# Optimization experiments

Hardware: AMD Instinct MI355X
Metric: run time of the kernel (lower is better)

Reference implementation:

```python
import jax, jax.numpy as jnp
import numpy as np

MARGIN = 0.3
EPS = 1e-8  # torch CosineSimilarity eps


def setup_inputs() -> dict:
    key = jax.random.key(0)
    k1, k2 = jax.random.split(key)
    x = jax.random.normal(k1, (8192, 1024), dtype=jnp.float32)
    y = jax.random.normal(k2, (8192, 1024), dtype=jnp.float32)
    return {"x": x, "y": y}


def _rank(S):
    # S[i, j] = cos(a_i, b_j); positives on the diagonal.
    d = jnp.diagonal(S)                      # [N] positive similarities
    E = jnp.exp(S)                           # [N, N]
    neg = jnp.sum(E, axis=1) - jnp.exp(d)    # sum over j != i of exp(S[i, j])
    m1 = jnp.exp(d - MARGIN)
    ret = -jnp.log(m1 / (m1 + neg))          # per-anchor AMS loss
    return jnp.mean(ret)


def reference(x, y):
    xn = x / jnp.maximum(jnp.linalg.norm(x, axis=-1, keepdims=True), EPS)
    yn = y / jnp.maximum(jnp.linalg.norm(y, axis=-1, keepdims=True), EPS)
    S = xn @ yn.T                            # [N, N] full cosine-similarity matrix
    # calculate_loss = rank(x, y) + rank(y, x); rank(y, x) uses S.T
    return _rank(S) + _rank(S.T)
```

## Files before the change

### kernel.cpp

```cpp
#include <hip/hip_runtime.h>
#include <hip/hip_bf16.h>
#include <math.h>

#define NROWS 8192
#define DDIM  1024
#define BT    128
#define BKB   128
#define MARGIN 0.3f
#define INV256 0.00390625f

typedef __attribute__((ext_vector_type(4))) float  f32x4;
typedef __attribute__((ext_vector_type(8))) __bf16 bf16x8;
typedef __attribute__((ext_vector_type(4))) int    i32x4;
typedef __attribute__((ext_vector_type(8))) int    i32x8;

__device__ __forceinline__ unsigned f2bf_bits(float f) {
  unsigned u = __float_as_uint(f);
  u += 0x7fffu + ((u >> 16) & 1u);
  return u >> 16;
}

__global__ __launch_bounds__(256) void normconv8_kernel(const float* __restrict__ x,
                                                        const float* __restrict__ y,
                                                        unsigned int* __restrict__ xq,
                                                        unsigned int* __restrict__ yq,
                                                        float* __restrict__ zero_base) {
  if (blockIdx.x < 16) {
    ((float4*)zero_base)[blockIdx.x * 256 + threadIdx.x] = (float4){0.f, 0.f, 0.f, 0.f};
  }
  int wid  = blockIdx.x * 4 + (threadIdx.x >> 6);
  int lane = threadIdx.x & 63;
  const float* src;
  unsigned int* dst;
  int row;
  if (wid < NROWS) { src = x; dst = xq; row = wid; }
  else             { src = y; dst = yq; row = wid - NROWS; }
  const float4* p = (const float4*)(src + (size_t)row * DDIM);
  float4 v[4];
  float s = 0.f;
#pragma unroll
  for (int a = 0; a < 4; ++a) {
    v[a] = p[a * 64 + lane];
    s = fmaf(v[a].x, v[a].x, s); s = fmaf(v[a].y, v[a].y, s);
    s = fmaf(v[a].z, v[a].z, s); s = fmaf(v[a].w, v[a].w, s);
  }
#pragma unroll
  for (int m = 1; m < 64; m <<= 1) s += __shfl_xor(s, m, 64);
  float inv = 16.0f / fmaxf(sqrtf(s), 1e-8f);
  unsigned int* d4 = dst + (size_t)row * (DDIM / 4);
#pragma unroll
  for (int a = 0; a < 4; ++a) {
    int w = __builtin_amdgcn_cvt_pk_fp8_f32(v[a].x * inv, v[a].y * inv, 0, false);
    w     = __builtin_amdgcn_cvt_pk_fp8_f32(v[a].z * inv, v[a].w * inv, w, true);
    d4[a * 64 + lane] = (unsigned int)w;
  }
}

__global__ __launch_bounds__(256) void gemm_mx_kernel(const unsigned char* __restrict__ xq,
                                                      const unsigned char* __restrict__ yq,
                                                      float* __restrict__ rowsum,
                                                      float* __restrict__ colsum,
                                                      float* __restrict__ diagv) {
  __shared__ alignas(16) unsigned char As[BT * BKB];
  __shared__ alignas(16) unsigned char Bs[BT * BKB];
  __shared__ float red_row[BT];
  __shared__ float red_col[BT];

  const int tid  = threadIdx.x;
  const int bi   = blockIdx.y;
  const int bj   = blockIdx.x;
  const int lane = tid & 63;
  const int wave = tid >> 6;
  const int wr   = wave >> 1, wc = wave & 1;
  const int quad = lane >> 4, l15 = lane & 15;

  if (tid < BT) red_row[tid] = 0.f; else red_col[tid - BT] = 0.f;

  const int r_l = lane >> 3;
  const int cg  = (lane & 7) ^ r_l;
  const unsigned char* ga = xq + (size_t)(bi * BT + wave * 32 + r_l) * DDIM + cg * 16;
  const unsigned char* gb = yq + (size_t)(bj * BT + wave * 32 + r_l) * DDIM + cg * 16;

  f32x4 acc[4][4];
#pragma unroll
  for (int i = 0; i < 4; ++i)
#pragma unroll
    for (int j = 0; j < 4; ++j) acc[i][j] = (f32x4){0.f, 0.f, 0.f, 0.f};

  const int r7 = l15 & 7;
  for (int k0 = 0; k0 < DDIM; k0 += BKB) {
#pragma unroll
    for (int a = 0; a < 4; ++a) {
      __builtin_amdgcn_global_load_lds(
          (const __attribute__((address_space(1))) unsigned int*)(ga + (size_t)a * 8 * DDIM + k0),
          (__attribute__((address_space(3))) unsigned int*)&As[(wave * 32 + a * 8) * BKB],
          16, 0, 0);
      __builtin_amdgcn_global_load_lds(
          (const __attribute__((address_space(1))) unsigned int*)(gb + (size_t)a * 8 * DDIM + k0),
          (__attribute__((address_space(3))) unsigned int*)&Bs[(wave * 32 + a * 8) * BKB],
          16, 0, 0);
    }
    __syncthreads();
    i32x8 af[4], bf[4];
#pragma unroll
    for (int f = 0; f < 4; ++f) {
      const unsigned char* ra = &As[(wr * 64 + f * 16 + l15) * BKB];
      const unsigned char* rb = &Bs[(wc * 64 + f * 16 + l15) * BKB];
      i32x4 alo = *(const i32x4*)(ra + (((quad * 2 + 0) ^ r7) * 16));
      i32x4 ahi = *(const i32x4*)(ra + (((quad * 2 + 1) ^ r7) * 16));
      i32x4 blo = *(const i32x4*)(rb + (((quad * 2 + 0) ^ r7) * 16));
      i32x4 bhi = *(const i32x4*)(rb + (((quad * 2 + 1) ^ r7) * 16));
      af[f] = (i32x8){alo.x, alo.y, alo.z, alo.w, ahi.x, ahi.y, ahi.z, ahi.w};
      bf[f] = (i32x8){blo.x, blo.y, blo.z, blo.w, bhi.x, bhi.y, bhi.z, bhi.w};
    }
#pragma unroll
    for (int fr = 0; fr < 4; ++fr)
#pragma unroll
      for (int fc = 0; fc < 4; ++fc)
        acc[fr][fc] = __builtin_amdgcn_mfma_scale_f32_16x16x128_f8f6f4(
            af[fr], bf[fc], acc[fr][fc],
            0, 0,
            0, 0x7F7F7F7F,
            0, 0x7F7F7F7F);
    __syncthreads();
  }

  if (bi == bj && wr == wc && (l15 >> 2) == quad) {
    int r = l15 & 3;
#pragma unroll
    for (int f = 0; f < 4; ++f)
      diagv[bi * BT + wr * 64 + f * 16 + l15] = acc[f][f][r] * INV256;
  }

  float racc[4][4];
  float cacc[4];
#pragma unroll
  for (int i = 0; i < 4; ++i) {
    cacc[i] = 0.f;
#pragma unroll
    for (int j = 0; j < 4; ++j) racc[i][j] = 0.f;
  }
#pragma unroll
  for (int fr = 0; fr < 4; ++fr)
#pragma unroll
    for (int fc = 0; fc < 4; ++fc) {
      f32x4 v = acc[fr][fc];
#pragma unroll
      for (int r = 0; r < 4; ++r) {
        float e = __expf(v[r] * INV256);
        racc[fr][r] += e;
        cacc[fc]    += e;
      }
    }
#pragma unroll
  for (int m = 1; m <= 8; m <<= 1)
#pragma unroll
    for (int fr = 0; fr < 4; ++fr)
#pragma unroll
      for (int r = 0; r < 4; ++r) racc[fr][r] += __shfl_xor(racc[fr][r], m, 64);
  if (l15 == 0)
#pragma unroll
    for (int fr = 0; fr < 4; ++fr)
#pragma unroll
      for (int r = 0; r < 4; ++r)
        atomicAdd(&red_row[wr * 64 + fr * 16 + quad * 4 + r], racc[fr][r]);
#pragma unroll
  for (int m = 16; m <= 32; m <<= 1)
#pragma unroll
    for (int fc = 0; fc < 4; ++fc) cacc[fc] += __shfl_xor(cacc[fc], m, 64);
  if (quad == 0)
#pragma unroll
    for (int fc = 0; fc < 4; ++fc)
      atomicAdd(&red_col[wc * 64 + fc * 16 + l15], cacc[fc]);

  __syncthreads();
  if (tid < BT) atomicAdd(&rowsum[bi * BT + tid], red_row[tid]);
  else          atomicAdd(&colsum[bj * BT + (tid - BT)], red_col[tid - BT]);
}

__global__ __launch_bounds__(256) void norm_kernel(const float* __restrict__ x,
                                                   const float* __restrict__ y,
                                                   float* __restrict__ invn) {
  int wid  = (int)((blockIdx.x * blockDim.x + threadIdx.x) >> 6);
  int lane = threadIdx.x & 63;
  const float* src = (wid < NROWS) ? x : y;
  int row = (wid < NROWS) ? wid : (wid - NROWS);
  const float4* p = (const float4*)(src + (size_t)row * DDIM);
  float s = 0.f;
#pragma unroll
  for (int a = 0; a < 4; ++a) {
    float4 v = p[a * 64 + lane];
    s = fmaf(v.x, v.x, s); s = fmaf(v.y, v.y, s);
    s = fmaf(v.z, v.z, s); s = fmaf(v.w, v.w, s);
  }
#pragma unroll
  for (int m = 1; m < 64; m <<= 1) s += __shfl_xor(s, m, 64);
  if (lane == 0) invn[wid] = 1.0f / fmaxf(sqrtf(s), 1e-8f);
}

__global__ __launch_bounds__(256) void gemm_kernel(const float* __restrict__ x,
                                                   const float* __restrict__ y,
                                                   const float* __restrict__ invn,
                                                   float* __restrict__ rowsum,
                                                   float* __restrict__ colsum,
                                                   float* __restrict__ diagv) {
  __shared__ alignas(16) unsigned short As[BT * 64];
  __shared__ alignas(16) unsigned short Bs[BT * 64];
  __shared__ float red_row[BT];
  __shared__ float red_col[BT];

  const int tid  = threadIdx.x;
  const int bi   = blockIdx.y;
  const int bj   = blockIdx.x;
  const int lane = tid & 63;
  const int wave = tid >> 6;
  const int wr   = wave >> 1, wc = wave & 1;
  const int quad = lane >> 4, l15 = lane & 15;
  const int srow = tid >> 4;
  const int sc4  = tid & 15;

  if (tid < BT) red_row[tid] = 0.f; else red_col[tid - BT] = 0.f;

  float ainv[8], binv[8];
#pragma unroll
  for (int a = 0; a < 8; ++a) {
    ainv[a] = invn[bi * BT + a * 16 + srow];
    binv[a] = invn[NROWS + bj * BT + a * 16 + srow];
  }

  f32x4 acc[4][4];
#pragma unroll
  for (int i = 0; i < 4; ++i)
#pragma unroll
    for (int j = 0; j < 4; ++j) acc[i][j] = (f32x4){0.f, 0.f, 0.f, 0.f};

  for (int k0 = 0; k0 < DDIM; k0 += 64) {
#pragma unroll
    for (int a = 0; a < 8; ++a) {
      int row = a * 16 + srow;
      float4 va = *(const float4*)(x + (size_t)(bi * BT + row) * DDIM + k0 + sc4 * 4);
      float4 vb = *(const float4*)(y + (size_t)(bj * BT + row) * DDIM + k0 + sc4 * 4);
      float sa = ainv[a], sb = binv[a];
      unsigned long long pa =
          (unsigned long long)f2bf_bits(va.x * sa) |
          ((unsigned long long)f2bf_bits(va.y * sa) << 16) |
          ((unsigned long long)f2bf_bits(va.z * sa) << 32) |
          ((unsigned long long)f2bf_bits(va.w * sa) << 48);
      unsigned long long pb =
          (unsigned long long)f2bf_bits(vb.x * sb) |
          ((unsigned long long)f2bf_bits(vb.y * sb) << 16) |
          ((unsigned long long)f2bf_bits(vb.z * sb) << 32) |
          ((unsigned long long)f2bf_bits(vb.w * sb) << 48);
      *(unsigned long long*)&As[row * 64 + sc4 * 4] = pa;
      *(unsigned long long*)&Bs[row * 64 + sc4 * 4] = pb;
    }
    __syncthreads();
#pragma unroll
    for (int kk = 0; kk < 64; kk += 32) {
      bf16x8 af[4], bf[4];
#pragma unroll
      for (int f = 0; f < 4; ++f) {
        af[f] = *(const bf16x8*)&As[(wr * 64 + f * 16 + l15) * 64 + kk + quad * 8];
        bf[f] = *(const bf16x8*)&Bs[(wc * 64 + f * 16 + l15) * 64 + kk + quad * 8];
      }
#pragma unroll
      for (int fr = 0; fr < 4; ++fr)
#pragma unroll
        for (int fc = 0; fc < 4; ++fc)
          acc[fr][fc] = __builtin_amdgcn_mfma_f32_16x16x32_bf16(af[fr], bf[fc], acc[fr][fc], 0, 0, 0);
    }
    __syncthreads();
  }

  if (bi == bj && wr == wc && (l15 >> 2) == quad) {
    int r = l15 & 3;
#pragma unroll
    for (int f = 0; f < 4; ++f)
      diagv[bi * BT + wr * 64 + f * 16 + l15] = acc[f][f][r];
  }

  float racc[4][4];
  float cacc[4];
#pragma unroll
  for (int i = 0; i < 4; ++i) {
    cacc[i] = 0.f;
#pragma unroll
    for (int j = 0; j < 4; ++j) racc[i][j] = 0.f;
  }
#pragma unroll
  for (int fr = 0; fr < 4; ++fr)
#pragma unroll
    for (int fc = 0; fc < 4; ++fc) {
      f32x4 v = acc[fr][fc];
#pragma unroll
      for (int r = 0; r < 4; ++r) {
        float e = __expf(v[r]);
        racc[fr][r] += e;
        cacc[fc]    += e;
      }
    }
#pragma unroll
  for (int m = 1; m <= 8; m <<= 1)
#pragma unroll
    for (int fr = 0; fr < 4; ++fr)
#pragma unroll
      for (int r = 0; r < 4; ++r) racc[fr][r] += __shfl_xor(racc[fr][r], m, 64);
  if (l15 == 0)
#pragma unroll
    for (int fr = 0; fr < 4; ++fr)
#pragma unroll
      for (int r = 0; r < 4; ++r)
        atomicAdd(&red_row[wr * 64 + fr * 16 + quad * 4 + r], racc[fr][r]);
#pragma unroll
  for (int m = 16; m <= 32; m <<= 1)
#pragma unroll
    for (int fc = 0; fc < 4; ++fc) cacc[fc] += __shfl_xor(cacc[fc], m, 64);
  if (quad == 0)
#pragma unroll
    for (int fc = 0; fc < 4; ++fc)
      atomicAdd(&red_col[wc * 64 + fc * 16 + l15], cacc[fc]);

  __syncthreads();
  if (tid < BT) atomicAdd(&rowsum[bi * BT + tid], red_row[tid]);
  else          atomicAdd(&colsum[bj * BT + (tid - BT)], red_col[tid - BT]);
}

__global__ __launch_bounds__(1024) void finalize_kernel(const float* __restrict__ rowsum,
                                                        const float* __restrict__ colsum,
                                                        const float* __restrict__ diagv,
                                                        float* __restrict__ out) {
  float s = 0.f;
  for (int i = threadIdx.x; i < NROWS; i += 1024) {
    float d  = diagv[i];
    float ed = __expf(d);
    float m1 = __expf(d - MARGIN);
    float negR = rowsum[i] - ed;
    float negC = colsum[i] - ed;
    s += __logf((m1 + negR) / m1) + __logf((m1 + negC) / m1);
  }
  __shared__ float red[16];
#pragma unroll
  for (int m = 1; m < 64; m <<= 1) s += __shfl_xor(s, m, 64);
  if ((threadIdx.x & 63) == 0) red[threadIdx.x >> 6] = s;
  __syncthreads();
  if (threadIdx.x < 64) {
    float v = (threadIdx.x < 16) ? red[threadIdx.x] : 0.f;
#pragma unroll
    for (int m = 1; m < 16; m <<= 1) v += __shfl_xor(v, m, 64);
    if (threadIdx.x == 0) out[0] = v / (float)NROWS;
  }
}

extern "C" void kernel_launch(void* const* d_in, const int* in_sizes, int n_in,
                              void* d_out, int out_size, void* d_ws, size_t ws_size,
                              hipStream_t stream) {
  const float* x = (const float*)d_in[0];
  const float* y = (const float*)d_in[1];
  float* out = (float*)d_out;
  char* ws = (char*)d_ws;

  const size_t q_bytes = (size_t)NROWS * DDIM;
  const size_t need_fast = 2 * q_bytes + 3 * NROWS * 4;

  if (ws_size >= need_fast) {
    unsigned int* xq = (unsigned int*)ws;
    unsigned int* yq = (unsigned int*)(ws + q_bytes);
    float* rowsum = (float*)(ws + 2 * q_bytes);
    float* colsum = rowsum + NROWS;
    float* diagv  = colsum + NROWS;
    normconv8_kernel<<<dim3((2 * NROWS) / 4), 256, 0, stream>>>(x, y, xq, yq, rowsum);
    gemm_mx_kernel<<<dim3(NROWS / BT, NROWS / BT), 256, 0, stream>>>(
        (const unsigned char*)xq, (const unsigned char*)yq, rowsum, colsum, diagv);
    finalize_kernel<<<dim3(1), 1024, 0, stream>>>(rowsum, colsum, diagv, out);
  } else {
    float* invn   = (float*)ws;
    float* rowsum = (float*)(ws + 16384 * 4);
    float* colsum = rowsum + NROWS;
    float* diagv  = colsum + NROWS;
    hipMemsetAsync(rowsum, 0, 2 * NROWS * sizeof(float), stream);
    norm_kernel<<<dim3((2 * NROWS) / 4 / 64), 256, 0, stream>>>(x, y, invn);
    gemm_kernel<<<dim3(NROWS / BT, NROWS / BT), 256, 0, stream>>>(x, y, invn, rowsum, colsum, diagv);
    finalize_kernel<<<dim3(1), 1024, 0, stream>>>(rowsum, colsum, diagv, out);
  }
}
```

Measured before the change: 190.7 us.

## Load A fragments directly from global and fuse finalize into GEMM via last-block counter

The A operand is no longer staged through LDS. Each lane loads its MFMA fragment straight from global memory, which halves LDS traffic and shared-memory footprint. The separate finalize kernel is removed: a global atomic counter lets the last GEMM block compute the final loss, saving one kernel launch. The risks are uncoalesced 32-byte A loads per lane with no reuse across the waves that share rows, plus serialized finalize work in a single block.

```diff
diff --git a/kernel.cpp b/kernel.cpp
--- a/kernel.cpp
+++ b/kernel.cpp
@@ -6,6 +6,7 @@
 #define DDIM  1024
 #define BT    128
 #define BKB   128
+#define NBLK  (NROWS / BT)
 #define MARGIN 0.3f
 #define INV256 0.00390625f
 
@@ -24,10 +25,12 @@
                                                         const float* __restrict__ y,
                                                         unsigned int* __restrict__ xq,
                                                         unsigned int* __restrict__ yq,
-                                                        float* __restrict__ zero_base) {
+                                                        float* __restrict__ zero_base,
+                                                        unsigned int* __restrict__ counter) {
   if (blockIdx.x < 16) {
     ((float4*)zero_base)[blockIdx.x * 256 + threadIdx.x] = (float4){0.f, 0.f, 0.f, 0.f};
   }
+  if (blockIdx.x == 16 && threadIdx.x == 0) *counter = 0u;
   int wid  = blockIdx.x * 4 + (threadIdx.x >> 6);
   int lane = threadIdx.x & 63;
   const float* src;
@@ -60,11 +63,13 @@
                                                       const unsigned char* __restrict__ yq,
                                                       float* __restrict__ rowsum,
                                                       float* __restrict__ colsum,
-                                                      float* __restrict__ diagv) {
-  __shared__ alignas(16) unsigned char As[BT * BKB];
+                                                      float* __restrict__ diagv,
+                                                      unsigned int* __restrict__ counter,
+                                                      float* __restrict__ out) {
   __shared__ alignas(16) unsigned char Bs[BT * BKB];
   __shared__ float red_row[BT];
   __shared__ float red_col[BT];
+  __shared__ int lastflag;
 
   const int tid  = threadIdx.x;
   const int bi   = blockIdx.y;
@@ -78,8 +83,12 @@
 
   const int r_l = lane >> 3;
   const int cg  = (lane & 7) ^ r_l;
-  const unsigned char* ga = xq + (size_t)(bi * BT + wave * 32 + r_l) * DDIM + cg * 16;
   const unsigned char* gb = yq + (size_t)(bj * BT + wave * 32 + r_l) * DDIM + cg * 16;
+
+  const unsigned char* arow[4];
+#pragma unroll
+  for (int f = 0; f < 4; ++f)
+    arow[f] = xq + (size_t)(bi * BT + wr * 64 + f * 16 + l15) * DDIM + quad * 32;
 
   f32x4 acc[4][4];
 #pragma unroll
@@ -91,26 +100,25 @@
   for (int k0 = 0; k0 < DDIM; k0 += BKB) {
 #pragma unroll
     for (int a = 0; a < 4; ++a) {
-      __builtin_amdgcn_global_load_lds(
-          (const __attribute__((address_space(1))) unsigned int*)(ga + (size_t)a * 8 * DDIM + k0),
-          (__attribute__((address_space(3))) unsigned int*)&As[(wave * 32 + a * 8) * BKB],
-          16, 0, 0);
       __builtin_amdgcn_global_load_lds(
           (const __attribute__((address_space(1))) unsigned int*)(gb + (size_t)a * 8 * DDIM + k0),
           (__attribute__((address_space(3))) unsigned int*)&Bs[(wave * 32 + a * 8) * BKB],
           16, 0, 0);
     }
+    i32x8 af[4];
+#pragma unroll
+    for (int f = 0; f < 4; ++f) {
+      i32x4 alo = *(const i32x4*)(arow[f] + k0);
+      i32x4 ahi = *(const i32x4*)(arow[f] + k0 + 16);
+      af[f] = (i32x8){alo.x, alo.y, alo.z, alo.w, ahi.x, ahi.y, ahi.z, ahi.w};
+    }
     __syncthreads();
-    i32x8 af[4], bf[4];
+    i32x8 bf[4];
 #pragma unroll
     for (int f = 0; f < 4; ++f) {
-      const unsigned char* ra = &As[(wr * 64 + f * 16 + l15) * BKB];
       const unsigned char* rb = &Bs[(wc * 64 + f * 16 + l15) * BKB];
-      i32x4 alo = *(const i32x4*)(ra + (((quad * 2 + 0) ^ r7) * 16));
-      i32x4 ahi = *(const i32x4*)(ra + (((quad * 2 + 1) ^ r7) * 16));
       i32x4 blo = *(const i32x4*)(rb + (((quad * 2 + 0) ^ r7) * 16));
       i32x4 bhi = *(const i32x4*)(rb + (((quad * 2 + 1) ^ r7) * 16));
-      af[f] = (i32x8){alo.x, alo.y, alo.z, alo.w, ahi.x, ahi.y, ahi.z, ahi.w};
       bf[f] = (i32x8){blo.x, blo.y, blo.z, blo.w, bhi.x, bhi.y, bhi.z, bhi.w};
     }
 #pragma unroll
@@ -129,7 +137,9 @@
     int r = l15 & 3;
 #pragma unroll
     for (int f = 0; f < 4; ++f)
-      diagv[bi * BT + wr * 64 + f * 16 + l15] = acc[f][f][r] * INV256;
+      __hip_atomic_store(&diagv[bi * BT + wr * 64 + f * 16 + l15],
+                         acc[f][f][r] * INV256,
+                         __ATOMIC_RELAXED, __HIP_MEMORY_SCOPE_AGENT);
   }
 
   float racc[4][4];
@@ -176,6 +186,31 @@
   __syncthreads();
   if (tid < BT) atomicAdd(&rowsum[bi * BT + tid], red_row[tid]);
   else          atomicAdd(&colsum[bj * BT + (tid - BT)], red_col[tid - BT]);
+
+  __threadfence();
+  if (tid == 0) {
+    unsigned int c = atomicAdd(counter, 1u);
+    lastflag = (c == (unsigned int)(NBLK * NBLK - 1));
+  }
+  __syncthreads();
+  if (lastflag) {
+    __threadfence();
+    float s = 0.f;
+    for (int i = tid; i < NROWS; i += 256) {
+      float d  = __hip_atomic_load(&diagv[i],  __ATOMIC_RELAXED, __HIP_MEMORY_SCOPE_AGENT);
+      float rs = __hip_atomic_load(&rowsum[i], __ATOMIC_RELAXED, __HIP_MEMORY_SCOPE_AGENT);
+      float cs = __hip_atomic_load(&colsum[i], __ATOMIC_RELAXED, __HIP_MEMORY_SCOPE_AGENT);
+      float ed = __expf(d);
+      float m1 = __expf(d - MARGIN);
+      s += __logf((m1 + (rs - ed)) / m1) + __logf((m1 + (cs - ed)) / m1);
+    }
+#pragma unroll
+    for (int m = 1; m < 64; m <<= 1) s += __shfl_xor(s, m, 64);
+    if ((tid & 63) == 0) red_row[tid >> 6] = s;
+    __syncthreads();
+    if (tid == 0)
+      out[0] = (red_row[0] + red_row[1] + red_row[2] + red_row[3]) / (float)NROWS;
+  }
 }
 
 __global__ __launch_bounds__(256) void norm_kernel(const float* __restrict__ x,
@@ -360,7 +395,7 @@
   char* ws = (char*)d_ws;
 
   const size_t q_bytes = (size_t)NROWS * DDIM;
-  const size_t need_fast = 2 * q_bytes + 3 * NROWS * 4;
+  const size_t need_fast = 2 * q_bytes + 3 * NROWS * 4 + 64;
 
   if (ws_size >= need_fast) {
     unsigned int* xq = (unsigned int*)ws;
@@ -368,10 +403,10 @@
     float* rowsum = (float*)(ws + 2 * q_bytes);
     float* colsum = rowsum + NROWS;
     float* diagv  = colsum + NROWS;
-    normconv8_kernel<<<dim3((2 * NROWS) / 4), 256, 0, stream>>>(x, y, xq, yq, rowsum);
-    gemm_mx_kernel<<<dim3(NROWS / BT, NROWS / BT), 256, 0, stream>>>(
-        (const unsigned char*)xq, (const unsigned char*)yq, rowsum, colsum, diagv);
-    finalize_kernel<<<dim3(1), 1024, 0, stream>>>(rowsum, colsum, diagv, out);
+    unsigned int* counter = (unsigned int*)(diagv + NROWS);
+    normconv8_kernel<<<dim3((2 * NROWS) / 4), 256, 0, stream>>>(x, y, xq, yq, rowsum, counter);
+    gemm_mx_kernel<<<dim3(NBLK, NBLK), 256, 0, stream>>>(
+        (const unsigned char*)xq, (const unsigned char*)yq, rowsum, colsum, diagv, counter, out);
   } else {
     float* invn   = (float*)ws;
     float* rowsum = (float*)(ws + 16384 * 4);
```

Result: slower. 481.8 us (+152.6%).
